# Performance work log

Measured on AMD Instinct MI355X. Metric: run time of the kernel, lower is better.

The kernel has to match this reference:

```python
import jax, jax.numpy as jnp
import numpy as np


def setup_inputs() -> dict:
    key = jax.random.key(0)
    k1, k2 = jax.random.split(key)
    H = W = 4096
    input1 = jax.random.normal(k1, (1, 1, H, W), dtype=jnp.float32)   # moving image
    input2 = jax.random.normal(k2, (1, 2, H, W), dtype=jnp.float32)   # dense flow (dH, dW)
    return {"input1": input1, "input2": input2}


def reference(input1, input2):
    # input1: [B=1, C=1, H, W] image; input2: [B=1, 2, H, W] displacement field
    B, C, H, W = input1.shape
    f32 = jnp.float32

    # identity mesh (matches torch.linspace outer-product construction)
    h_mesh = jnp.broadcast_to(jnp.arange(H, dtype=f32)[None, :, None], (B, H, W))
    w_mesh = jnp.broadcast_to(jnp.arange(W, dtype=f32)[None, None, :], (B, H, W))

    # warped sampling coordinates, shifted by +1 for the zero-padding border
    H_up = (input2[:, 0] + h_mesh).reshape(-1) + 1.0   # [B*H*W]
    W_up = (input2[:, 1] + w_mesh).reshape(-1) + 1.0

    # zero-pad image by 1 pixel on each spatial side
    img = jnp.pad(input1, ((0, 0), (0, 0), (1, 1), (1, 1)))  # [B, C, H+2, W+2]
    Hp, Wp = H + 2, W + 2

    hf = jnp.floor(H_up).astype(jnp.int32)
    hc = hf + 1
    wf = jnp.floor(W_up).astype(jnp.int32)
    wc = wf + 1
    hf = jnp.clip(hf, 0, Hp - 1)
    hc = jnp.clip(hc, 0, Hp - 1)
    wf = jnp.clip(wf, 0, Wp - 1)
    wc = jnp.clip(wc, 0, Wp - 1)

    img_flat = img.reshape(-1)  # B = C = 1
    val_000 = img_flat[hf * Wp + wf]
    val_010 = img_flat[hc * Wp + wf]
    val_001 = img_flat[hf * Wp + wc]
    val_011 = img_flat[hc * Wp + wc]

    dH = hc.astype(f32) - H_up
    dW = wc.astype(f32) - W_up
    out = (val_000 * (dW * dH)
           + val_010 * (dW * (1.0 - dH))
           + val_001 * ((1.0 - dW) * dH)
           + val_011 * ((1.0 - dW) * (1.0 - dH)))

    # [B*H*W] -> [B, H, W, C] -> [B, C, H, W]
    return out.reshape(B, H, W, C).transpose(0, 3, 1, 2)
```

## Files before the change

kernel.cpp:

```cpp
#include <hip/hip_runtime.h>


#define IMG_H 4096
#define IMG_W 4096
#define TR 16
#define TC 128
#define HALO 8
#define SR (TR + 2 * HALO)
#define SC (TC + 2 * HALO)
#define SC4 (SC / 4)
#define NCHUNK (SR * SC4)

typedef float f2  __attribute__((ext_vector_type(2)));
typedef float f2u __attribute__((ext_vector_type(2), aligned(4)));
typedef float f4  __attribute__((ext_vector_type(4)));

__global__ __launch_bounds__(256) void warp_bilinear_kernel(
    const float* __restrict__ img,
    const float* __restrict__ flow,
    float* __restrict__ out)
{
    __shared__ float tile[SR * SC];

    const int HW   = IMG_H * IMG_W;
    const int tid  = threadIdx.x;
    const int lane = tid & 63;
    const int wv   = tid >> 6;
    const int w0   = blockIdx.x * TC + lane * 2;
    const int h0   = blockIdx.y * TR + wv * 4;
    const int r_lo = blockIdx.y * TR - HALO;
    const int c_lo = blockIdx.x * TC - HALO;

    #pragma unroll
    for (int it = 0; it < 5; ++it) {
        int t = tid + it * 256;
        if (t < NCHUNK) {
            int i  = t / SC4;
            int m  = t - i * SC4;
            int gr = min(max(r_lo + i, 0), IMG_H - 1);
            int gc = min(max(c_lo + 4 * m, 0), IMG_W - 4);
            f4 v = *(const f4*)(img + gr * IMG_W + gc);
            *(f4*)(tile + i * SC + 4 * m) = v;
        }
    }

    int rowidx[4];
    f2  fh[4], fw[4];
    #pragma unroll
    for (int r = 0; r < 4; ++r)
        rowidx[r] = (h0 + r) * IMG_W + w0;
    #pragma unroll
    for (int r = 0; r < 4; ++r)
        fh[r] = __builtin_nontemporal_load((const f2*)(flow + rowidx[r]));
    #pragma unroll
    for (int r = 0; r < 4; ++r)
        fw[r] = __builtin_nontemporal_load((const f2*)(flow + HW + rowidx[r]));

    __syncthreads();

    #pragma unroll
    for (int g = 0; g < 2; ++g) {
        int   li0[2][2], li1[2][2];
        int   ob0[2][2], ob1[2][2];
        float a0x[2][2], a0y[2][2], a1x[2][2], a1y[2][2];
        bool  ok = true;

        #pragma unroll
        for (int rr = 0; rr < 2; ++rr) {
            const int r = 2 * g + rr;
            #pragma unroll
            for (int c = 0; c < 2; ++c) {
                const int h = h0 + r;
                const int w = w0 + c;
                float Hu = (fh[r][c] + (float)h) + 1.0f;
                float Wu = (fw[r][c] + (float)w) + 1.0f;

                int hf = (int)floorf(Hu);
                int wf = (int)floorf(Wu);
                int hc = hf + 1;
                int wc = wf + 1;

                int hfc = min(max(hf, 0), IMG_H + 1);
                int hcc = min(max(hc, 0), IMG_H + 1);
                int wfc = min(max(wf, 0), IMG_W + 1);
                int wcc = min(max(wc, 0), IMG_W + 1);

                float dH = (float)hcc - Hu;
                float dW = (float)wcc - Wu;

                int rf = hfc - 1, rc = hcc - 1, cf = wfc - 1, cc = wcc - 1;
                bool rf_in = (unsigned)rf < IMG_H;
                bool rc_in = (unsigned)rc < IMG_H;
                bool cf_in = (unsigned)cf < IMG_W;
                bool cc_in = (unsigned)cc < IMG_W;

                int rf_cl = min(max(rf, 0), IMG_H - 1);
                int rc_cl = min(max(rc, 0), IMG_H - 1);
                int cf_cl = min(max(cf, 0), IMG_W - 1);
                int cc_cl = min(max(cc, 0), IMG_W - 1);
                int cb    = min(max(cf, 0), IMG_W - 2);

                int sf = cf_cl - cb;
                int sc = cc_cl - cb;

                int i0 = rf_cl - r_lo;
                int i1 = rc_cl - r_lo;
                int jb = cb - c_lo;
                ok = ok && ((unsigned)i0 < SR) && ((unsigned)i1 < SR)
                        && ((unsigned)jb < (SC - 1));
                li0[rr][c] = i0 * SC + jb;
                li1[rr][c] = i1 * SC + jb;
                ob0[rr][c] = (rf_cl << 12) + cb;
                ob1[rr][c] = (rc_cl << 12) + cb;

                float A = dW * dH;
                float B = dW * (1.0f - dH);
                float C = (1.0f - dW) * dH;
                float D = (1.0f - dW) * (1.0f - dH);
                float w00 = (rf_in && cf_in) ? A : 0.0f;
                float w10 = (rc_in && cf_in) ? B : 0.0f;
                float w01 = (rf_in && cc_in) ? C : 0.0f;
                float w11 = (rc_in && cc_in) ? D : 0.0f;

                a0x[rr][c] = (sf ? 0.0f : w00) + (sc ? 0.0f : w01);
                a0y[rr][c] = (sf ? w00 : 0.0f) + (sc ? w01 : 0.0f);
                a1x[rr][c] = (sf ? 0.0f : w10) + (sc ? 0.0f : w11);
                a1y[rr][c] = (sf ? w10 : 0.0f) + (sc ? w11 : 0.0f);
            }
        }

        float q0x[2][2], q0y[2][2], q1x[2][2], q1y[2][2];
        if (__builtin_expect(ok, 1)) {
            #pragma unroll
            for (int rr = 0; rr < 2; ++rr)
                #pragma unroll
                for (int c = 0; c < 2; ++c) {
                    q0x[rr][c] = tile[li0[rr][c]];
                    q0y[rr][c] = tile[li0[rr][c] + 1];
                    q1x[rr][c] = tile[li1[rr][c]];
                    q1y[rr][c] = tile[li1[rr][c] + 1];
                }
        } else {
            #pragma unroll
            for (int rr = 0; rr < 2; ++rr)
                #pragma unroll
                for (int c = 0; c < 2; ++c) {
                    f2u p0 = *(const f2u*)(img + ob0[rr][c]);
                    f2u p1 = *(const f2u*)(img + ob1[rr][c]);
                    q0x[rr][c] = p0.x; q0y[rr][c] = p0.y;
                    q1x[rr][c] = p1.x; q1y[rr][c] = p1.y;
                }
        }

        #pragma unroll
        for (int rr = 0; rr < 2; ++rr) {
            f2 res;
            #pragma unroll
            for (int c = 0; c < 2; ++c) {
                res[c] = q0x[rr][c] * a0x[rr][c] + q0y[rr][c] * a0y[rr][c]
                       + q1x[rr][c] * a1x[rr][c] + q1y[rr][c] * a1y[rr][c];
            }
            __builtin_nontemporal_store(res, (f2*)(out + rowidx[2 * g + rr]));
        }
    }
}

extern "C" void kernel_launch(void* const* d_in, const int* in_sizes, int n_in,
                              void* d_out, int out_size, void* d_ws, size_t ws_size,
                              hipStream_t stream) {
    const float* img  = (const float*)d_in[0];
    const float* flow = (const float*)d_in[1];
    float* out = (float*)d_out;

    dim3 grid(IMG_W / TC, IMG_H / TR);
    dim3 block(256);
    warp_bilinear_kernel<<<grid, block, 0, stream>>>(img, flow, out);
}
```

Measured before the change: 239.1 us.

## Split border blocks to a global path and simplify interior bilinear math

Blocks on the image border skip the shared-memory tile load and compute every pixel with clamped global loads through a helper. Interior blocks drop the clamping and border-validity logic: because tile bounds checks guarantee in-range indices, weights and tile indices come straight from floor values. All four rows are processed in one batch, which raises instruction-level parallelism at the cost of more live registers. The intent is to reduce ALU work per pixel in this memory-bound kernel.

```diff
diff --git a/kernel.cpp b/kernel.cpp
--- a/kernel.cpp
+++ b/kernel.cpp
@@ -15,6 +15,59 @@
 typedef float f2u __attribute__((ext_vector_type(2), aligned(4)));
 typedef float f4  __attribute__((ext_vector_type(4)));
 
+__device__ __forceinline__ float full_pixel(const float* __restrict__ img,
+                                            float fhv, float fwv, int h, int w)
+{
+    float Hu = (fhv + (float)h) + 1.0f;
+    float Wu = (fwv + (float)w) + 1.0f;
+
+    int hf = (int)floorf(Hu);
+    int wf = (int)floorf(Wu);
+    int hc = hf + 1;
+    int wc = wf + 1;
+
+    int hfc = min(max(hf, 0), IMG_H + 1);
+    int hcc = min(max(hc, 0), IMG_H + 1);
+    int wfc = min(max(wf, 0), IMG_W + 1);
+    int wcc = min(max(wc, 0), IMG_W + 1);
+
+    float dH = (float)hcc - Hu;
+    float dW = (float)wcc - Wu;
+
+    int rf = hfc - 1, rc = hcc - 1, cf = wfc - 1, cc = wcc - 1;
+    bool rf_in = (unsigned)rf < IMG_H;
+    bool rc_in = (unsigned)rc < IMG_H;
+    bool cf_in = (unsigned)cf < IMG_W;
+    bool cc_in = (unsigned)cc < IMG_W;
+
+    int rf_cl = min(max(rf, 0), IMG_H - 1);
+    int rc_cl = min(max(rc, 0), IMG_H - 1);
+    int cf_cl = min(max(cf, 0), IMG_W - 1);
+    int cc_cl = min(max(cc, 0), IMG_W - 1);
+    int cb    = min(max(cf, 0), IMG_W - 2);
+
+    int sf = cf_cl - cb;
+    int sc = cc_cl - cb;
+
+    float A = dW * dH;
+    float B = dW * (1.0f - dH);
+    float C = (1.0f - dW) * dH;
+    float D = (1.0f - dW) * (1.0f - dH);
+    float w00 = (rf_in && cf_in) ? A : 0.0f;
+    float w10 = (rc_in && cf_in) ? B : 0.0f;
+    float w01 = (rf_in && cc_in) ? C : 0.0f;
+    float w11 = (rc_in && cc_in) ? D : 0.0f;
+
+    float a0x = (sf ? 0.0f : w00) + (sc ? 0.0f : w01);
+    float a0y = (sf ? w00 : 0.0f) + (sc ? w01 : 0.0f);
+    float a1x = (sf ? 0.0f : w10) + (sc ? 0.0f : w11);
+    float a1y = (sf ? w10 : 0.0f) + (sc ? w11 : 0.0f);
+
+    f2u p0 = *(const f2u*)(img + (rf_cl << 12) + cb);
+    f2u p1 = *(const f2u*)(img + (rc_cl << 12) + cb);
+    return p0.x * a0x + p0.y * a0y + p1.x * a1x + p1.y * a1y;
+}
+
 __global__ __launch_bounds__(256) void warp_bilinear_kernel(
     const float* __restrict__ img,
     const float* __restrict__ flow,
@@ -26,23 +79,14 @@
     const int tid  = threadIdx.x;
     const int lane = tid & 63;
     const int wv   = tid >> 6;
-    const int w0   = blockIdx.x * TC + lane * 2;
-    const int h0   = blockIdx.y * TR + wv * 4;
-    const int r_lo = blockIdx.y * TR - HALO;
-    const int c_lo = blockIdx.x * TC - HALO;
-
-    #pragma unroll
-    for (int it = 0; it < 5; ++it) {
-        int t = tid + it * 256;
-        if (t < NCHUNK) {
-            int i  = t / SC4;
-            int m  = t - i * SC4;
-            int gr = min(max(r_lo + i, 0), IMG_H - 1);
-            int gc = min(max(c_lo + 4 * m, 0), IMG_W - 4);
-            f4 v = *(const f4*)(img + gr * IMG_W + gc);
-            *(f4*)(tile + i * SC + 4 * m) = v;
-        }
-    }
+    const int bx   = blockIdx.x, by = blockIdx.y;
+    const int w0   = bx * TC + lane * 2;
+    const int h0   = by * TR + wv * 4;
+    const int r_lo = by * TR - HALO;
+    const int c_lo = bx * TC - HALO;
+
+    const bool border = (bx == 0) | (bx == gridDim.x - 1) |
+                        (by == 0) | (by == gridDim.y - 1);
 
     int rowidx[4];
     f2  fh[4], fw[4];
@@ -56,112 +100,98 @@
     for (int r = 0; r < 4; ++r)
         fw[r] = __builtin_nontemporal_load((const f2*)(flow + HW + rowidx[r]));
 
-    __syncthreads();
-
-    #pragma unroll
-    for (int g = 0; g < 2; ++g) {
-        int   li0[2][2], li1[2][2];
-        int   ob0[2][2], ob1[2][2];
-        float a0x[2][2], a0y[2][2], a1x[2][2], a1y[2][2];
-        bool  ok = true;
-
-        #pragma unroll
-        for (int rr = 0; rr < 2; ++rr) {
-            const int r = 2 * g + rr;
-            #pragma unroll
-            for (int c = 0; c < 2; ++c) {
-                const int h = h0 + r;
-                const int w = w0 + c;
-                float Hu = (fh[r][c] + (float)h) + 1.0f;
-                float Wu = (fw[r][c] + (float)w) + 1.0f;
-
-                int hf = (int)floorf(Hu);
-                int wf = (int)floorf(Wu);
-                int hc = hf + 1;
-                int wc = wf + 1;
-
-                int hfc = min(max(hf, 0), IMG_H + 1);
-                int hcc = min(max(hc, 0), IMG_H + 1);
-                int wfc = min(max(wf, 0), IMG_W + 1);
-                int wcc = min(max(wc, 0), IMG_W + 1);
-
-                float dH = (float)hcc - Hu;
-                float dW = (float)wcc - Wu;
-
-                int rf = hfc - 1, rc = hcc - 1, cf = wfc - 1, cc = wcc - 1;
-                bool rf_in = (unsigned)rf < IMG_H;
-                bool rc_in = (unsigned)rc < IMG_H;
-                bool cf_in = (unsigned)cf < IMG_W;
-                bool cc_in = (unsigned)cc < IMG_W;
-
-                int rf_cl = min(max(rf, 0), IMG_H - 1);
-                int rc_cl = min(max(rc, 0), IMG_H - 1);
-                int cf_cl = min(max(cf, 0), IMG_W - 1);
-                int cc_cl = min(max(cc, 0), IMG_W - 1);
-                int cb    = min(max(cf, 0), IMG_W - 2);
-
-                int sf = cf_cl - cb;
-                int sc = cc_cl - cb;
-
-                int i0 = rf_cl - r_lo;
-                int i1 = rc_cl - r_lo;
-                int jb = cb - c_lo;
-                ok = ok && ((unsigned)i0 < SR) && ((unsigned)i1 < SR)
-                        && ((unsigned)jb < (SC - 1));
-                li0[rr][c] = i0 * SC + jb;
-                li1[rr][c] = i1 * SC + jb;
-                ob0[rr][c] = (rf_cl << 12) + cb;
-                ob1[rr][c] = (rc_cl << 12) + cb;
-
-                float A = dW * dH;
-                float B = dW * (1.0f - dH);
-                float C = (1.0f - dW) * dH;
-                float D = (1.0f - dW) * (1.0f - dH);
-                float w00 = (rf_in && cf_in) ? A : 0.0f;
-                float w10 = (rc_in && cf_in) ? B : 0.0f;
-                float w01 = (rf_in && cc_in) ? C : 0.0f;
-                float w11 = (rc_in && cc_in) ? D : 0.0f;
-
-                a0x[rr][c] = (sf ? 0.0f : w00) + (sc ? 0.0f : w01);
-                a0y[rr][c] = (sf ? w00 : 0.0f) + (sc ? w01 : 0.0f);
-                a1x[rr][c] = (sf ? 0.0f : w10) + (sc ? 0.0f : w11);
-                a1y[rr][c] = (sf ? w10 : 0.0f) + (sc ? w11 : 0.0f);
+    if (!border) {
+        #pragma unroll
+        for (int it = 0; it < 5; ++it) {
+            int t = tid + it * 256;
+            if (t < NCHUNK) {
+                int i  = t / SC4;
+                int m  = t - i * SC4;
+                int gr = min(max(r_lo + i, 0), IMG_H - 1);
+                int gc = min(max(c_lo + 4 * m, 0), IMG_W - 4);
+                f4 v = *(const f4*)(img + gr * IMG_W + gc);
+                *(f4*)(tile + i * SC + 4 * m) = v;
             }
         }
-
-        float q0x[2][2], q0y[2][2], q1x[2][2], q1y[2][2];
-        if (__builtin_expect(ok, 1)) {
-            #pragma unroll
-            for (int rr = 0; rr < 2; ++rr)
-                #pragma unroll
-                for (int c = 0; c < 2; ++c) {
-                    q0x[rr][c] = tile[li0[rr][c]];
-                    q0y[rr][c] = tile[li0[rr][c] + 1];
-                    q1x[rr][c] = tile[li1[rr][c]];
-                    q1y[rr][c] = tile[li1[rr][c] + 1];
-                }
-        } else {
-            #pragma unroll
-            for (int rr = 0; rr < 2; ++rr)
-                #pragma unroll
-                for (int c = 0; c < 2; ++c) {
-                    f2u p0 = *(const f2u*)(img + ob0[rr][c]);
-                    f2u p1 = *(const f2u*)(img + ob1[rr][c]);
-                    q0x[rr][c] = p0.x; q0y[rr][c] = p0.y;
-                    q1x[rr][c] = p1.x; q1y[rr][c] = p1.y;
-                }
+    }
+    __syncthreads();
+
+    if (border) {
+        #pragma unroll
+        for (int r = 0; r < 4; ++r) {
+            f2 res;
+            #pragma unroll
+            for (int c = 0; c < 2; ++c)
+                res[c] = full_pixel(img, fh[r][c], fw[r][c], h0 + r, w0 + c);
+            __builtin_nontemporal_store(res, (f2*)(out + rowidx[r]));
         }
-
-        #pragma unroll
-        for (int rr = 0; rr < 2; ++rr) {
-            f2 res;
+        return;
+    }
+
+    int   li0[4][2], li1[4][2];
+    float A_[4][2], B_[4][2], C_[4][2], D_[4][2];
+    bool  ok = true;
+    const int rbase = -1 - r_lo;
+    const int cbase = -1 - c_lo;
+
+    #pragma unroll
+    for (int r = 0; r < 4; ++r) {
+        #pragma unroll
+        for (int c = 0; c < 2; ++c) {
+            float Hu = (fh[r][c] + (float)(h0 + r)) + 1.0f;
+            float Wu = (fw[r][c] + (float)(w0 + c)) + 1.0f;
+
+            int hf = (int)floorf(Hu);
+            int wf = (int)floorf(Wu);
+            float dH = (float)(hf + 1) - Hu;
+            float dW = (float)(wf + 1) - Wu;
+
+            int i0 = hf + rbase;
+            int jb = wf + cbase;
+            ok = ok && ((unsigned)i0 < SR - 1) && ((unsigned)jb < SC - 1);
+            li0[r][c] = i0 * SC + jb;
+            li1[r][c] = li0[r][c] + SC;
+
+            float omH = 1.0f - dH, omW = 1.0f - dW;
+            A_[r][c] = dW * dH;
+            C_[r][c] = omW * dH;
+            B_[r][c] = dW * omH;
+            D_[r][c] = omW * omH;
+        }
+    }
+
+    float res[4][2];
+    if (__builtin_expect(ok, 1)) {
+        float q0x[4][2], q0y[4][2], q1x[4][2], q1y[4][2];
+        #pragma unroll
+        for (int r = 0; r < 4; ++r)
             #pragma unroll
             for (int c = 0; c < 2; ++c) {
-                res[c] = q0x[rr][c] * a0x[rr][c] + q0y[rr][c] * a0y[rr][c]
-                       + q1x[rr][c] * a1x[rr][c] + q1y[rr][c] * a1y[rr][c];
+                q0x[r][c] = tile[li0[r][c]];
+                q0y[r][c] = tile[li0[r][c] + 1];
+                q1x[r][c] = tile[li1[r][c]];
+                q1y[r][c] = tile[li1[r][c] + 1];
             }
-            __builtin_nontemporal_store(res, (f2*)(out + rowidx[2 * g + rr]));
-        }
+        #pragma unroll
+        for (int r = 0; r < 4; ++r)
+            #pragma unroll
+            for (int c = 0; c < 2; ++c)
+                res[r][c] = q0x[r][c] * A_[r][c] + q0y[r][c] * C_[r][c]
+                          + q1x[r][c] * B_[r][c] + q1y[r][c] * D_[r][c];
+    }
+    if (__builtin_expect(!ok, 0)) {
+        #pragma unroll
+        for (int r = 0; r < 4; ++r)
+            #pragma unroll
+            for (int c = 0; c < 2; ++c)
+                res[r][c] = full_pixel(img, fh[r][c], fw[r][c],
+                                       h0 + r, w0 + c);
+    }
+
+    #pragma unroll
+    for (int r = 0; r < 4; ++r) {
+        f2 v; v[0] = res[r][0]; v[1] = res[r][1];
+        __builtin_nontemporal_store(v, (f2*)(out + rowidx[r]));
     }
 }
 
```

After: 254.8 us. 6.6% more time.
